# Kernel tuning notes

Hardware: AMD Instinct MI355X
Metric: run time of the kernel (lower is better)

The kernel has to match this reference:

```python
import jax, jax.numpy as jnp
import numpy as np

DIM = 2048
HEADS = 16
DIM_HEAD = 128
DIM_INNER = HEADS * DIM_HEAD  # 2048
EPS = 1.1920929e-07  # torch RMSNorm default eps = finfo(float32).eps


def setup_inputs() -> dict:
    key = jax.random.key(0)
    k_tok, k_q, k_kv, k_o = jax.random.split(key, 4)
    tokens = jax.random.normal(k_tok, (4, 2048, DIM), dtype=jnp.float32)
    # Linear weights stored as [in, out]; torch init ~ U(-1/sqrt(in), 1/sqrt(in)), use scaled normal
    s = 0.02
    w_q = jax.random.normal(k_q, (DIM, DIM_INNER), dtype=jnp.float32) * s
    w_kv = jax.random.normal(k_kv, (DIM, 2 * DIM_INNER), dtype=jnp.float32) * s
    w_out = jax.random.normal(k_o, (DIM_INNER, DIM), dtype=jnp.float32) * s
    norm_weight = jnp.ones((DIM,), dtype=jnp.float32)
    return {"tokens": tokens, "norm_weight": norm_weight, "w_q": w_q, "w_kv": w_kv, "w_out": w_out}


def _rmsnorm(x, weight):
    var = jnp.mean(jnp.square(x), axis=-1, keepdims=True)
    return x * jax.lax.rsqrt(var + EPS) * weight


def reference(tokens, norm_weight, w_q, w_kv, w_out):
    b, n, _ = tokens.shape
    x = _rmsnorm(tokens, norm_weight)
    q = x @ w_q                       # [b, n, h*d]
    kv = x @ w_kv                     # [b, n, 2*h*d]
    k, v = jnp.split(kv, 2, axis=-1)

    def split_heads(t):
        return t.reshape(b, n, HEADS, DIM_HEAD).transpose(0, 2, 1, 3)  # b h n d

    q, k, v = map(split_heads, (q, k, v))
    q = q * (DIM_HEAD ** -0.5)
    sim = jnp.einsum('bhid,bhjd->bhij', q, k)
    attn = jax.nn.softmax(sim, axis=-1)
    out = jnp.einsum('bhij,bhjd->bhid', attn, v)
    out = out.transpose(0, 2, 1, 3).reshape(b, n, DIM_INNER)
    return out @ w_out
```

## Files before the change

### kernel.cpp

```cpp
#include <hip/hip_runtime.h>
#include <hip/hip_bf16.h>
#include <stdint.h>

#define SEQ   2048
#define DIM   2048
#define HEADS 16
#define DHEAD 128
#define BATCH 4
#define MROWS (BATCH*SEQ)

typedef short bf16x8 __attribute__((ext_vector_type(8)));
typedef float f32x4  __attribute__((ext_vector_type(4)));
typedef float f32x16 __attribute__((ext_vector_type(16)));
typedef unsigned short u16x8 __attribute__((ext_vector_type(8)));
typedef unsigned int u32x4 __attribute__((ext_vector_type(4)));

__device__ __forceinline__ short f2bf(float f){
  union { float fv; unsigned u; } x; x.fv = f;
  unsigned r = x.u + 0x7fffu + ((x.u >> 16) & 1u);
  return (short)(r >> 16);
}

__device__ __forceinline__ unsigned cvtpk(float lo, float hi){
  unsigned r; asm("v_cvt_pk_bf16_f32 %0, %1, %2" : "=v"(r) : "v"(lo), "v"(hi)); return r;
}

__device__ __forceinline__ float exp2a(float x){
#if __has_builtin(__builtin_amdgcn_exp2f)
  return __builtin_amdgcn_exp2f(x);
#else
  return exp2f(x);
#endif
}

__device__ __forceinline__ void gl_lds16(const void* g, void* l){
  __builtin_amdgcn_global_load_lds((const __attribute__((address_space(1))) void*)g,
                                   (__attribute__((address_space(3))) void*)l, 16, 0, 0);
}

__global__ __launch_bounds__(256) void rmsnorm_cast_k(const float* __restrict__ tok,
                                                      const float* __restrict__ w,
                                                      short* __restrict__ x){
  const int row = blockIdx.x;
  const float4* r4 = (const float4*)(tok + (size_t)row * DIM);
  float4 a = r4[threadIdx.x * 2];
  float4 b = r4[threadIdx.x * 2 + 1];
  float ss = a.x*a.x + a.y*a.y + a.z*a.z + a.w*a.w
           + b.x*b.x + b.y*b.y + b.z*b.z + b.w*b.w;
  #pragma unroll
  for (int m = 1; m < 64; m <<= 1) ss += __shfl_xor(ss, m, 64);
  __shared__ float red[4];
  if ((threadIdx.x & 63) == 0) red[threadIdx.x >> 6] = ss;
  __syncthreads();
  float tot = red[0] + red[1] + red[2] + red[3];
  float rs = rsqrtf(tot * (1.0f / DIM) + 1.1920929e-07f);
  const float4* w4 = (const float4*)w;
  float4 wa = w4[threadIdx.x * 2];
  float4 wb = w4[threadIdx.x * 2 + 1];
  u16x8 o;
  o[0] = (unsigned short)f2bf(a.x * rs * wa.x);
  o[1] = (unsigned short)f2bf(a.y * rs * wa.y);
  o[2] = (unsigned short)f2bf(a.z * rs * wa.z);
  o[3] = (unsigned short)f2bf(a.w * rs * wa.w);
  o[4] = (unsigned short)f2bf(b.x * rs * wb.x);
  o[5] = (unsigned short)f2bf(b.y * rs * wb.y);
  o[6] = (unsigned short)f2bf(b.z * rs * wb.z);
  o[7] = (unsigned short)f2bf(b.w * rs * wb.w);
  *(u16x8*)(x + (size_t)row * DIM + threadIdx.x * 8) = o;
}

__global__ __launch_bounds__(256) void wtrans_k(const float* __restrict__ w,
                                                short* __restrict__ wt,
                                                int K, int N){
  __shared__ float tile[64][65];
  const int r0 = blockIdx.y * 64;
  const int c0 = blockIdx.x * 64;
  const int t = threadIdx.x;
  #pragma unroll
  for (int i = 0; i < 16; i++){
    int e = i * 256 + t; int r = e >> 6, c = e & 63;
    tile[r][c] = w[(size_t)(r0 + r) * N + c0 + c];
  }
  __syncthreads();
  #pragma unroll
  for (int i = 0; i < 16; i++){
    int e = i * 256 + t; int c = e >> 6, r = e & 63;
    wt[(size_t)(c0 + c) * K + r0 + r] = f2bf(tile[r][c]);
  }
}

__global__ __launch_bounds__(256) void vtrans_k(const short* __restrict__ kv,
                                                short* __restrict__ vt){
  __shared__ short tile[64][65];
  const int n0 = blockIdx.x * 64;
  const int d0 = blockIdx.y * 64;
  const int bh = blockIdx.z;
  const int b = bh >> 4, h = bh & 15;
  const int t = threadIdx.x;
  #pragma unroll
  for (int i = 0; i < 16; i++){
    int e = i * 256 + t; int r = e >> 6, c = e & 63;
    tile[r][c] = kv[(size_t)(b * SEQ + n0 + r) * 4096 + 2048 + h * DHEAD + d0 + c];
  }
  __syncthreads();
  #pragma unroll
  for (int i = 0; i < 16; i++){
    int e = i * 256 + t; int c = e >> 6, r = e & 63;
    vt[(size_t)(bh * DHEAD + d0 + c) * SEQ + n0 + r] = tile[r][c];
  }
}

__device__ __forceinline__ void storeC(float* C, size_t idx, float v){ C[idx] = v; }
__device__ __forceinline__ void storeC(short* C, size_t idx, float v){ C[idx] = f2bf(v); }

template<typename OutT>
__global__ __launch_bounds__(512, 2) void gemm256_k(const short* __restrict__ A,
                                                    const short* __restrict__ Bt,
                                                    OutT* __restrict__ C,
                                                    int M, int N, int K, int lgntn){
  __shared__ __align__(16) short As[4][256 * 32];
  __shared__ __align__(16) short Bs[4][256 * 32];
  const int nwg = gridDim.x;
  const int bid = blockIdx.x;
  const int o = (bid & 7) * (nwg >> 3) + (bid >> 3);
  const int bm = o >> lgntn, bn = o & ((1 << lgntn) - 1);
  const int m0 = bm << 8, n0 = bn << 8;
  const int tid = threadIdx.x, lane = tid & 63, wid = tid >> 6;
  const int l31 = lane & 31, hi = lane >> 5;
  const int wr = wid >> 2, wc = wid & 3;
  const int NT = K >> 5;

  f32x16 acc[4][2] = {};

  auto stage = [&](int t){
    const int slot = t & 3;
    const size_t kbase = (size_t)t << 5;
    #pragma unroll
    for (int i = 0; i < 2; i++){
      int c = i * 512 + tid;
      int row = c >> 2;
      int j = (c & 3) ^ ((row >> 1) & 3);
      gl_lds16(A + (size_t)(m0 + row) * K + kbase + j * 8,
               &As[slot][(i * 512 + wid * 64) * 8]);
    }
    #pragma unroll
    for (int i = 0; i < 2; i++){
      int c = i * 512 + tid;
      int row = c >> 2;
      int j = (c & 3) ^ ((row >> 1) & 3);
      gl_lds16(Bt + (size_t)(n0 + row) * K + kbase + j * 8,
               &Bs[slot][(i * 512 + wid * 64) * 8]);
    }
  };

  auto compute = [&](int t){
    const short* Ab = As[t & 3];
    const short* Bb = Bs[t & 3];
    bf16x8 af[4][2], bfv[2][2];
    #pragma unroll
    for (int mb = 0; mb < 4; mb++){
      int row = wr * 128 + mb * 32 + l31;
      #pragma unroll
      for (int ks = 0; ks < 2; ks++){
        int ch = (ks * 2 + hi) ^ ((row >> 1) & 3);
        af[mb][ks] = *(const bf16x8*)&Ab[row * 32 + ch * 8];
      }
    }
    #pragma unroll
    for (int nb = 0; nb < 2; nb++){
      int row = wc * 64 + nb * 32 + l31;
      #pragma unroll
      for (int ks = 0; ks < 2; ks++){
        int ch = (ks * 2 + hi) ^ ((row >> 1) & 3);
        bfv[nb][ks] = *(const bf16x8*)&Bb[row * 32 + ch * 8];
      }
    }
    __builtin_amdgcn_s_setprio(1);
    #pragma unroll
    for (int mb = 0; mb < 4; mb++)
      #pragma unroll
      for (int nb = 0; nb < 2; nb++)
        #pragma unroll
        for (int ks = 0; ks < 2; ks++)
          acc[mb][nb] = __builtin_amdgcn_mfma_f32_32x32x16_bf16(af[mb][ks], bfv[nb][ks],
                                                                acc[mb][nb], 0, 0, 0);
    __builtin_amdgcn_s_setprio(0);
  };

  stage(0); stage(1); stage(2);
  asm volatile("s_waitcnt vmcnt(8)" ::: "memory");
  __builtin_amdgcn_s_barrier();

  for (int t = 0; t < NT; t++){
    if (t + 3 < NT) stage(t + 3);
    compute(t);
    if (t + 1 < NT){
      if (t + 3 < NT)      asm volatile("s_waitcnt vmcnt(8)" ::: "memory");
      else if (t + 2 < NT) asm volatile("s_waitcnt vmcnt(4)" ::: "memory");
      else                 asm volatile("s_waitcnt vmcnt(0)" ::: "memory");
      __builtin_amdgcn_s_barrier();
    }
  }

  #pragma unroll
  for (int mb = 0; mb < 4; mb++)
    #pragma unroll
    for (int nb = 0; nb < 2; nb++)
      #pragma unroll
      for (int reg = 0; reg < 16; reg++){
        int r = (reg & 3) + 8 * (reg >> 2) + 4 * hi;
        int row = m0 + wr * 128 + mb * 32 + r;
        int col = n0 + wc * 64 + nb * 32 + l31;
        storeC(C, (size_t)row * N + col, acc[mb][nb][reg]);
      }
}

__global__ __launch_bounds__(256) void attn_k(const short* __restrict__ q,
                                              const short* __restrict__ kv,
                                              const short* __restrict__ vt,
                                              short* __restrict__ out){
  __shared__ __align__(16) short Ks[2][64 * 128];
  __shared__ __align__(16) short Vts[2][128 * 64];
  const int qt = blockIdx.x, bh = blockIdx.y;
  const int b = bh >> 4, h = bh & 15;
  const int tid = threadIdx.x, lane = tid & 63, wid = tid >> 6;
  const int l31 = lane & 31, hi = lane >> 5;
  const int qrow0 = qt * 128 + wid * 32;
  const float c2 = 0.08838834764831845f * 1.4426950408889634f;
  const int NT = SEQ / 64;

  bf16x8 qf[8];
  {
    const short* qp = q + (size_t)(b * SEQ + qrow0 + l31) * DIM + h * DHEAD + hi * 8;
    #pragma unroll
    for (int s = 0; s < 8; s++) qf[s] = *(const bf16x8*)(qp + s * 16);
  }

  f32x16 acc[4] = {};
  float m2 = -3e38f, l_s = 0.f;

  auto stage = [&](int kt, int bs){
    #pragma unroll
    for (int i = 0; i < 4; i++){
      int cb = (i * 4 + wid) * 64;
      int c  = cb + lane;
      int kr = c >> 4, kj = (c & 15) ^ (kr & 7);
      gl_lds16(kv + (size_t)(b * SEQ + kt * 64 + kr) * 4096 + h * DHEAD + kj * 8,
               &Ks[bs][cb * 8]);
      int vr = c >> 3, vj = (c & 7) ^ (vr & 7);
      gl_lds16(vt + (size_t)(bh * DHEAD + vr) * SEQ + kt * 64 + vj * 8,
               &Vts[bs][cb * 8]);
    }
  };

  stage(0, 0);
  int cur = 0;

  for (int kt = 0; kt < NT; kt++){
    if (kt + 1 < NT){
      stage(kt + 1, cur ^ 1);
      asm volatile("s_waitcnt vmcnt(8)" ::: "memory");
    } else {
      asm volatile("s_waitcnt vmcnt(0)" ::: "memory");
    }
    __builtin_amdgcn_s_barrier();

    const short* Kb = Ks[cur];
    const short* Vb = Vts[cur];

    f32x16 t0 = {0,0,0,0,0,0,0,0,0,0,0,0,0,0,0,0};
    f32x16 t1 = t0;
    {
      const int r0 = l31, r1 = l31 + 32;
      #pragma unroll
      for (int s = 0; s < 8; s++){
        bf16x8 k0 = *(const bf16x8*)&Kb[r0 * 128 + (((2 * s + hi) ^ (r0 & 7)) * 8)];
        bf16x8 k1 = *(const bf16x8*)&Kb[r1 * 128 + (((2 * s + hi) ^ (r1 & 7)) * 8)];
        t0 = __builtin_amdgcn_mfma_f32_32x32x16_bf16(k0, qf[s], t0, 0, 0, 0);
        t1 = __builtin_amdgcn_mfma_f32_32x32x16_bf16(k1, qf[s], t1, 0, 0, 0);
      }
    }

    float mxr = t0[0];
    #pragma unroll
    for (int i = 1; i < 16; i++) mxr = fmaxf(mxr, t0[i]);
    #pragma unroll
    for (int i = 0; i < 16; i++) mxr = fmaxf(mxr, t1[i]);
    mxr = fmaxf(mxr, __shfl_xor(mxr, 32));
    float mx2 = mxr * c2;
    if (!__all(mx2 <= m2 + 11.5f)){
      float m2n = fmaxf(m2, mx2);
      float al = exp2a(m2 - m2n);
      m2 = m2n;
      l_s *= al;
      #pragma unroll
      for (int reg = 0; reg < 16; reg++){
        float ar = __shfl(al, (reg & 3) + 8 * (reg >> 2) + 4 * hi);
        #pragma unroll
        for (int dt = 0; dt < 4; dt++) acc[dt][reg] *= ar;
      }
    }

    float ps = 0.f;
    unsigned w[16];
    #pragma unroll
    for (int pr = 0; pr < 8; pr++){
      float pa_ = exp2a(fmaf(t0[2 * pr], c2, -m2));
      float pb_ = exp2a(fmaf(t0[2 * pr + 1], c2, -m2));
      ps += pa_ + pb_;
      w[pr] = cvtpk(pa_, pb_);
    }
    #pragma unroll
    for (int pr = 0; pr < 8; pr++){
      float pa_ = exp2a(fmaf(t1[2 * pr], c2, -m2));
      float pb_ = exp2a(fmaf(t1[2 * pr + 1], c2, -m2));
      ps += pa_ + pb_;
      w[8 + pr] = cvtpk(pa_, pb_);
    }
    ps += __shfl_xor(ps, 32);
    l_s += ps;

    #pragma unroll
    for (int fp = 0; fp < 4; fp++){
      unsigned A0 = w[fp * 4 + 0], A1 = w[fp * 4 + 1];
      unsigned B0 = w[fp * 4 + 2], B1 = w[fp * 4 + 3];
      unsigned xA0 = __shfl_xor((int)A0, 32), xA1 = __shfl_xor((int)A1, 32);
      unsigned xB0 = __shfl_xor((int)B0, 32), xB1 = __shfl_xor((int)B1, 32);
      u32x4 fw;
      fw[0] = hi ? xB0 : A0;
      fw[1] = hi ? xB1 : A1;
      fw[2] = hi ? B0 : xA0;
      fw[3] = hi ? B1 : xA1;
      union { u32x4 u; bf16x8 v; } pc; pc.u = fw;
      #pragma unroll
      for (int dt = 0; dt < 4; dt++){
        int vr = dt * 32 + l31;
        bf16x8 vb = *(const bf16x8*)&Vb[vr * 64 + (((2 * fp + hi) ^ (vr & 7)) * 8)];
        acc[dt] = __builtin_amdgcn_mfma_f32_32x32x16_bf16(pc.v, vb, acc[dt], 0, 0, 0);
      }
    }

    asm volatile("s_waitcnt lgkmcnt(0)" ::: "memory");
    __builtin_amdgcn_s_barrier();
    cur ^= 1;
  }

  float inv = 1.0f / l_s;
  #pragma unroll
  for (int reg = 0; reg < 16; reg++){
    int cr = (reg & 3) + 8 * (reg >> 2) + 4 * hi;
    float li = __shfl(inv, cr);
    int row = qrow0 + cr;
    #pragma unroll
    for (int dt = 0; dt < 4; dt++)
      out[(size_t)(b * SEQ + row) * DIM + h * DHEAD + dt * 32 + l31] = f2bf(acc[dt][reg] * li);
  }
}

extern "C" void kernel_launch(void* const* d_in, const int* in_sizes, int n_in,
                              void* d_out, int out_size, void* d_ws, size_t ws_size,
                              hipStream_t stream) {
  (void)in_sizes; (void)n_in; (void)out_size; (void)ws_size;
  const float* tokens = (const float*)d_in[0];
  const float* normw  = (const float*)d_in[1];
  const float* wq     = (const float*)d_in[2];
  const float* wkv    = (const float*)d_in[3];
  const float* wout   = (const float*)d_in[4];
  float* outp = (float*)d_out;
  char* ws = (char*)d_ws;

  short* x     = (short*)(ws + 0);
  short* wqt   = (short*)(ws + 33554432);
  short* wkvt  = (short*)(ws + 41943040);
  short* woutt = (short*)(ws + 58720256);
  short* qb    = (short*)(ws + 67108864);
  short* kvb   = (short*)(ws + 100663296);
  short* vtb   = (short*)(ws + 167772160);

  rmsnorm_cast_k<<<dim3(MROWS), dim3(256), 0, stream>>>(tokens, normw, x);
  wtrans_k<<<dim3(2048/64, 2048/64), dim3(256), 0, stream>>>(wq,   wqt,   2048, 2048);
  wtrans_k<<<dim3(4096/64, 2048/64), dim3(256), 0, stream>>>(wkv,  wkvt,  2048, 4096);
  wtrans_k<<<dim3(2048/64, 2048/64), dim3(256), 0, stream>>>(wout, woutt, 2048, 2048);
  gemm256_k<short><<<dim3((MROWS/256)*(2048/256)), dim3(512), 0, stream>>>(x, wqt,  qb,  MROWS, 2048, 2048, 3);
  gemm256_k<short><<<dim3((MROWS/256)*(4096/256)), dim3(512), 0, stream>>>(x, wkvt, kvb, MROWS, 4096, 2048, 4);
  vtrans_k<<<dim3(SEQ/64, DHEAD/64, BATCH*HEADS), dim3(256), 0, stream>>>(kvb, vtb);
  attn_k<<<dim3(SEQ/128, BATCH*HEADS), dim3(256), 0, stream>>>(qb, kvb, vtb, qb);
  gemm256_k<float><<<dim3((MROWS/256)*(2048/256)), dim3(512), 0, stream>>>(qb, woutt, outp, MROWS, 2048, 2048, 3);
}
```

Measured before the change: 610.9 us.

## Restage attention K/V loads with single-buffered V and add scheduling fences

The attention loop now loads the current V tile at the start of each iteration and prefetches the next K tile, with V kept in a single LDS buffer. The wait-and-barrier moves to just before the PV MFMAs, so V loads overlap the QK product and softmax. This cuts attention LDS use, which could allow more resident blocks, in exchange for a full vmcnt(0) drain at the end of each iteration. Separately, sched_barrier fences are added around GEMM and attention staging, the row-max becomes a tree reduction, and the exp sums are split across four accumulators to shorten dependency chains.

Result: slower. 649.3 us (+6.3%).

```diff
diff --git a/kernel.cpp b/kernel.cpp
--- a/kernel.cpp
+++ b/kernel.cpp
@@ -36,6 +36,11 @@
 __device__ __forceinline__ void gl_lds16(const void* g, void* l){
   __builtin_amdgcn_global_load_lds((const __attribute__((address_space(1))) void*)g,
                                    (__attribute__((address_space(3))) void*)l, 16, 0, 0);
+}
+
+__device__ __forceinline__ void ofence(){
+  asm volatile("" ::: "memory");
+  __builtin_amdgcn_sched_barrier(0);
 }
 
 __global__ __launch_bounds__(256) void rmsnorm_cast_k(const float* __restrict__ tok,
@@ -187,12 +192,14 @@
     __builtin_amdgcn_s_setprio(0);
   };
 
-  stage(0); stage(1); stage(2);
+  stage(0); ofence();
+  stage(1); ofence();
+  stage(2); ofence();
   asm volatile("s_waitcnt vmcnt(8)" ::: "memory");
   __builtin_amdgcn_s_barrier();
 
   for (int t = 0; t < NT; t++){
-    if (t + 3 < NT) stage(t + 3);
+    if (t + 3 < NT){ stage(t + 3); ofence(); }
     compute(t);
     if (t + 1 < NT){
       if (t + 3 < NT)      asm volatile("s_waitcnt vmcnt(8)" ::: "memory");
@@ -220,7 +227,7 @@
                                               const short* __restrict__ vt,
                                               short* __restrict__ out){
   __shared__ __align__(16) short Ks[2][64 * 128];
-  __shared__ __align__(16) short Vts[2][128 * 64];
+  __shared__ __align__(16) short Vts[128 * 64];
   const int qt = blockIdx.x, bh = blockIdx.y;
   const int b = bh >> 4, h = bh & 15;
   const int tid = threadIdx.x, lane = tid & 63, wid = tid >> 6;
@@ -235,11 +242,12 @@
     #pragma unroll
     for (int s = 0; s < 8; s++) qf[s] = *(const bf16x8*)(qp + s * 16);
   }
+  ofence();
 
   f32x16 acc[4] = {};
   float m2 = -3e38f, l_s = 0.f;
 
-  auto stage = [&](int kt, int bs){
+  auto stage_K = [&](int kt, int bs){
     #pragma unroll
     for (int i = 0; i < 4; i++){
       int cb = (i * 4 + wid) * 64;
@@ -247,26 +255,31 @@
       int kr = c >> 4, kj = (c & 15) ^ (kr & 7);
       gl_lds16(kv + (size_t)(b * SEQ + kt * 64 + kr) * 4096 + h * DHEAD + kj * 8,
                &Ks[bs][cb * 8]);
+    }
+  };
+  auto stage_V = [&](int kt){
+    #pragma unroll
+    for (int i = 0; i < 4; i++){
+      int cb = (i * 4 + wid) * 64;
+      int c  = cb + lane;
       int vr = c >> 3, vj = (c & 7) ^ (vr & 7);
       gl_lds16(vt + (size_t)(bh * DHEAD + vr) * SEQ + kt * 64 + vj * 8,
-               &Vts[bs][cb * 8]);
+               &Vts[cb * 8]);
     }
   };
 
-  stage(0, 0);
-  int cur = 0;
+  stage_K(0, 0); ofence();
 
   for (int kt = 0; kt < NT; kt++){
-    if (kt + 1 < NT){
-      stage(kt + 1, cur ^ 1);
+    const int cur = kt & 1;
+    stage_V(kt); ofence();
+    if (kt + 1 < NT){ stage_K(kt + 1, cur ^ 1); ofence(); }
+    if (kt == 0){
       asm volatile("s_waitcnt vmcnt(8)" ::: "memory");
-    } else {
-      asm volatile("s_waitcnt vmcnt(0)" ::: "memory");
-    }
-    __builtin_amdgcn_s_barrier();
+      __builtin_amdgcn_s_barrier();
+    }
 
     const short* Kb = Ks[cur];
-    const short* Vb = Vts[cur];
 
     f32x16 t0 = {0,0,0,0,0,0,0,0,0,0,0,0,0,0,0,0};
     f32x16 t1 = t0;
@@ -281,12 +294,15 @@
       }
     }
 
-    float mxr = t0[0];
-    #pragma unroll
-    for (int i = 1; i < 16; i++) mxr = fmaxf(mxr, t0[i]);
-    #pragma unroll
-    for (int i = 0; i < 16; i++) mxr = fmaxf(mxr, t1[i]);
-    mxr = fmaxf(mxr, __shfl_xor(mxr, 32));
+    float mr[8];
+    #pragma unroll
+    for (int i = 0; i < 8; i++)
+      mr[i] = fmaxf(fmaxf(t0[i], t0[i + 8]), fmaxf(t1[i], t1[i + 8]));
+    #pragma unroll
+    for (int s = 4; s > 0; s >>= 1)
+      #pragma unroll
+      for (int i = 0; i < s; i++) mr[i] = fmaxf(mr[i], mr[i + s]);
+    float mxr = fmaxf(mr[0], __shfl_xor(mr[0], 32));
     float mx2 = mxr * c2;
     if (!__all(mx2 <= m2 + 11.5f)){
       float m2n = fmaxf(m2, mx2);
@@ -301,24 +317,29 @@
       }
     }
 
-    float ps = 0.f;
+    float ps0 = 0.f, ps1 = 0.f, ps2 = 0.f, ps3 = 0.f;
     unsigned w[16];
     #pragma unroll
     for (int pr = 0; pr < 8; pr++){
       float pa_ = exp2a(fmaf(t0[2 * pr], c2, -m2));
       float pb_ = exp2a(fmaf(t0[2 * pr + 1], c2, -m2));
-      ps += pa_ + pb_;
+      ps0 += pa_; ps1 += pb_;
       w[pr] = cvtpk(pa_, pb_);
     }
     #pragma unroll
     for (int pr = 0; pr < 8; pr++){
       float pa_ = exp2a(fmaf(t1[2 * pr], c2, -m2));
       float pb_ = exp2a(fmaf(t1[2 * pr + 1], c2, -m2));
-      ps += pa_ + pb_;
+      ps2 += pa_; ps3 += pb_;
       w[8 + pr] = cvtpk(pa_, pb_);
     }
+    float ps = (ps0 + ps1) + (ps2 + ps3);
     ps += __shfl_xor(ps, 32);
     l_s += ps;
+
+    if (kt + 1 < NT) asm volatile("s_waitcnt vmcnt(4)" ::: "memory");
+    else             asm volatile("s_waitcnt vmcnt(0)" ::: "memory");
+    __builtin_amdgcn_s_barrier();
 
     #pragma unroll
     for (int fp = 0; fp < 4; fp++){
@@ -335,14 +356,13 @@
       #pragma unroll
       for (int dt = 0; dt < 4; dt++){
         int vr = dt * 32 + l31;
-        bf16x8 vb = *(const bf16x8*)&Vb[vr * 64 + (((2 * fp + hi) ^ (vr & 7)) * 8)];
+        bf16x8 vb = *(const bf16x8*)&Vts[vr * 64 + (((2 * fp + hi) ^ (vr & 7)) * 8)];
         acc[dt] = __builtin_amdgcn_mfma_f32_32x32x16_bf16(pc.v, vb, acc[dt], 0, 0, 0);
       }
     }
 
-    asm volatile("s_waitcnt lgkmcnt(0)" ::: "memory");
+    asm volatile("s_waitcnt vmcnt(0) lgkmcnt(0)" ::: "memory");
     __builtin_amdgcn_s_barrier();
-    cur ^= 1;
   }
 
   float inv = 1.0f / l_s;
```

## Process two query tiles per wave in attention to share K/V fragment loads

Applied to the files above, without the earlier changes.

Each attention wave now handles 64 query rows as two 32-row tiles. Every K and V fragment read from LDS feeds two MFMA chains, which halves LDS traffic per unit of matrix work. The online softmax now runs per 32-key subtile for each query tile, and the grid is halved to match. Scheduling barriers are also added around the async stage loads in the GEMM and attention kernels to pin instruction order. The cost is much higher register use (two sets of accumulators and Q fragments) and half as many blocks, which may lower occupancy or cause spills.

Result: slower. 624.0 us (+2.1%).

```diff
diff --git a/kernel.cpp b/kernel.cpp
--- a/kernel.cpp
+++ b/kernel.cpp
@@ -36,6 +36,11 @@
 __device__ __forceinline__ void gl_lds16(const void* g, void* l){
   __builtin_amdgcn_global_load_lds((const __attribute__((address_space(1))) void*)g,
                                    (__attribute__((address_space(3))) void*)l, 16, 0, 0);
+}
+
+__device__ __forceinline__ void ofence(){
+  asm volatile("" ::: "memory");
+  __builtin_amdgcn_sched_barrier(0);
 }
 
 __global__ __launch_bounds__(256) void rmsnorm_cast_k(const float* __restrict__ tok,
@@ -187,12 +192,14 @@
     __builtin_amdgcn_s_setprio(0);
   };
 
-  stage(0); stage(1); stage(2);
+  stage(0); ofence();
+  stage(1); ofence();
+  stage(2); ofence();
   asm volatile("s_waitcnt vmcnt(8)" ::: "memory");
   __builtin_amdgcn_s_barrier();
 
   for (int t = 0; t < NT; t++){
-    if (t + 3 < NT) stage(t + 3);
+    if (t + 3 < NT){ stage(t + 3); ofence(); }
     compute(t);
     if (t + 1 < NT){
       if (t + 3 < NT)      asm volatile("s_waitcnt vmcnt(8)" ::: "memory");
@@ -225,19 +232,22 @@
   const int b = bh >> 4, h = bh & 15;
   const int tid = threadIdx.x, lane = tid & 63, wid = tid >> 6;
   const int l31 = lane & 31, hi = lane >> 5;
-  const int qrow0 = qt * 128 + wid * 32;
+  const int qrow0 = qt * 256 + wid * 64;
   const float c2 = 0.08838834764831845f * 1.4426950408889634f;
   const int NT = SEQ / 64;
 
-  bf16x8 qf[8];
+  bf16x8 qfA[8], qfB[8];
   {
-    const short* qp = q + (size_t)(b * SEQ + qrow0 + l31) * DIM + h * DHEAD + hi * 8;
-    #pragma unroll
-    for (int s = 0; s < 8; s++) qf[s] = *(const bf16x8*)(qp + s * 16);
-  }
-
-  f32x16 acc[4] = {};
-  float m2 = -3e38f, l_s = 0.f;
+    const short* qpA = q + (size_t)(b * SEQ + qrow0 + l31) * DIM + h * DHEAD + hi * 8;
+    const short* qpB = qpA + (size_t)32 * DIM;
+    #pragma unroll
+    for (int s = 0; s < 8; s++){ qfA[s] = *(const bf16x8*)(qpA + s * 16);
+                                 qfB[s] = *(const bf16x8*)(qpB + s * 16); }
+  }
+  ofence();
+
+  f32x16 accA[4] = {}, accB[4] = {};
+  float m2A = -3e38f, lA = 0.f, m2B = -3e38f, lB = 0.f;
 
   auto stage = [&](int kt, int bs){
     #pragma unroll
@@ -253,12 +263,47 @@
     }
   };
 
-  stage(0, 0);
-  int cur = 0;
+  auto smpack = [&](f32x16& t, float& m2r, float& lr, f32x16* acc_, unsigned* wv){
+    float mr[8];
+    #pragma unroll
+    for (int i = 0; i < 8; i++) mr[i] = fmaxf(t[i], t[i + 8]);
+    #pragma unroll
+    for (int s = 4; s > 0; s >>= 1)
+      #pragma unroll
+      for (int i = 0; i < s; i++) mr[i] = fmaxf(mr[i], mr[i + s]);
+    float mxr = fmaxf(mr[0], __shfl_xor(mr[0], 32));
+    float mx2 = mxr * c2;
+    if (!__all(mx2 <= m2r + 11.5f)){
+      float m2n = fmaxf(m2r, mx2);
+      float al = exp2a(m2r - m2n);
+      m2r = m2n;
+      lr *= al;
+      #pragma unroll
+      for (int reg = 0; reg < 16; reg++){
+        float ar = __shfl(al, (reg & 3) + 8 * (reg >> 2) + 4 * hi);
+        #pragma unroll
+        for (int dt = 0; dt < 4; dt++) acc_[dt][reg] *= ar;
+      }
+    }
+    float p0 = 0.f, p1 = 0.f;
+    #pragma unroll
+    for (int pr = 0; pr < 8; pr++){
+      float pa_ = exp2a(fmaf(t[2 * pr], c2, -m2r));
+      float pb_ = exp2a(fmaf(t[2 * pr + 1], c2, -m2r));
+      p0 += pa_; p1 += pb_;
+      wv[pr] = cvtpk(pa_, pb_);
+    }
+    float ps = p0 + p1;
+    ps += __shfl_xor(ps, 32);
+    lr += ps;
+  };
+
+  stage(0, 0); ofence();
 
   for (int kt = 0; kt < NT; kt++){
+    const int cur = kt & 1;
     if (kt + 1 < NT){
-      stage(kt + 1, cur ^ 1);
+      stage(kt + 1, cur ^ 1); ofence();
       asm volatile("s_waitcnt vmcnt(8)" ::: "memory");
     } else {
       asm volatile("s_waitcnt vmcnt(0)" ::: "memory");
@@ -268,92 +313,72 @@
     const short* Kb = Ks[cur];
     const short* Vb = Vts[cur];
 
-    f32x16 t0 = {0,0,0,0,0,0,0,0,0,0,0,0,0,0,0,0};
-    f32x16 t1 = t0;
-    {
-      const int r0 = l31, r1 = l31 + 32;
-      #pragma unroll
-      for (int s = 0; s < 8; s++){
-        bf16x8 k0 = *(const bf16x8*)&Kb[r0 * 128 + (((2 * s + hi) ^ (r0 & 7)) * 8)];
-        bf16x8 k1 = *(const bf16x8*)&Kb[r1 * 128 + (((2 * s + hi) ^ (r1 & 7)) * 8)];
-        t0 = __builtin_amdgcn_mfma_f32_32x32x16_bf16(k0, qf[s], t0, 0, 0, 0);
-        t1 = __builtin_amdgcn_mfma_f32_32x32x16_bf16(k1, qf[s], t1, 0, 0, 0);
-      }
-    }
-
-    float mxr = t0[0];
-    #pragma unroll
-    for (int i = 1; i < 16; i++) mxr = fmaxf(mxr, t0[i]);
-    #pragma unroll
-    for (int i = 0; i < 16; i++) mxr = fmaxf(mxr, t1[i]);
-    mxr = fmaxf(mxr, __shfl_xor(mxr, 32));
-    float mx2 = mxr * c2;
-    if (!__all(mx2 <= m2 + 11.5f)){
-      float m2n = fmaxf(m2, mx2);
-      float al = exp2a(m2 - m2n);
-      m2 = m2n;
-      l_s *= al;
-      #pragma unroll
-      for (int reg = 0; reg < 16; reg++){
-        float ar = __shfl(al, (reg & 3) + 8 * (reg >> 2) + 4 * hi);
+    #pragma unroll
+    for (int ksub = 0; ksub < 2; ksub++){
+      f32x16 tA = {0,0,0,0,0,0,0,0,0,0,0,0,0,0,0,0};
+      f32x16 tB = tA;
+      {
+        const int r = ksub * 32 + l31;
+        __builtin_amdgcn_s_setprio(1);
         #pragma unroll
-        for (int dt = 0; dt < 4; dt++) acc[dt][reg] *= ar;
-      }
-    }
-
-    float ps = 0.f;
-    unsigned w[16];
-    #pragma unroll
-    for (int pr = 0; pr < 8; pr++){
-      float pa_ = exp2a(fmaf(t0[2 * pr], c2, -m2));
-      float pb_ = exp2a(fmaf(t0[2 * pr + 1], c2, -m2));
-      ps += pa_ + pb_;
-      w[pr] = cvtpk(pa_, pb_);
-    }
-    #pragma unroll
-    for (int pr = 0; pr < 8; pr++){
-      float pa_ = exp2a(fmaf(t1[2 * pr], c2, -m2));
-      float pb_ = exp2a(fmaf(t1[2 * pr + 1], c2, -m2));
-      ps += pa_ + pb_;
-      w[8 + pr] = cvtpk(pa_, pb_);
-    }
-    ps += __shfl_xor(ps, 32);
-    l_s += ps;
-
-    #pragma unroll
-    for (int fp = 0; fp < 4; fp++){
-      unsigned A0 = w[fp * 4 + 0], A1 = w[fp * 4 + 1];
-      unsigned B0 = w[fp * 4 + 2], B1 = w[fp * 4 + 3];
-      unsigned xA0 = __shfl_xor((int)A0, 32), xA1 = __shfl_xor((int)A1, 32);
-      unsigned xB0 = __shfl_xor((int)B0, 32), xB1 = __shfl_xor((int)B1, 32);
-      u32x4 fw;
-      fw[0] = hi ? xB0 : A0;
-      fw[1] = hi ? xB1 : A1;
-      fw[2] = hi ? B0 : xA0;
-      fw[3] = hi ? B1 : xA1;
-      union { u32x4 u; bf16x8 v; } pc; pc.u = fw;
-      #pragma unroll
-      for (int dt = 0; dt < 4; dt++){
-        int vr = dt * 32 + l31;
-        bf16x8 vb = *(const bf16x8*)&Vb[vr * 64 + (((2 * fp + hi) ^ (vr & 7)) * 8)];
-        acc[dt] = __builtin_amdgcn_mfma_f32_32x32x16_bf16(pc.v, vb, acc[dt], 0, 0, 0);
+        for (int s = 0; s < 8; s++){
+          bf16x8 k = *(const bf16x8*)&Kb[r * 128 + (((2 * s + hi) ^ (r & 7)) * 8)];
+          tA = __builtin_amdgcn_mfma_f32_32x32x16_bf16(k, qfA[s], tA, 0, 0, 0);
+          tB = __builtin_amdgcn_mfma_f32_32x32x16_bf16(k, qfB[s], tB, 0, 0, 0);
+        }
+        __builtin_amdgcn_s_setprio(0);
+      }
+
+      unsigned wA[8], wB[8];
+      smpack(tA, m2A, lA, accA, wA);
+      smpack(tB, m2B, lB, accB, wB);
+
+      #pragma unroll
+      for (int fpl = 0; fpl < 2; fpl++){
+        unsigned A0 = wA[fpl * 4 + 0], A1 = wA[fpl * 4 + 1];
+        unsigned B0 = wA[fpl * 4 + 2], B1 = wA[fpl * 4 + 3];
+        unsigned xA0 = __shfl_xor((int)A0, 32), xA1 = __shfl_xor((int)A1, 32);
+        unsigned xB0 = __shfl_xor((int)B0, 32), xB1 = __shfl_xor((int)B1, 32);
+        u32x4 fwA;
+        fwA[0] = hi ? xB0 : A0;  fwA[1] = hi ? xB1 : A1;
+        fwA[2] = hi ? B0 : xA0;  fwA[3] = hi ? B1 : xA1;
+        unsigned C0 = wB[fpl * 4 + 0], C1 = wB[fpl * 4 + 1];
+        unsigned D0 = wB[fpl * 4 + 2], D1 = wB[fpl * 4 + 3];
+        unsigned xC0 = __shfl_xor((int)C0, 32), xC1 = __shfl_xor((int)C1, 32);
+        unsigned xD0 = __shfl_xor((int)D0, 32), xD1 = __shfl_xor((int)D1, 32);
+        u32x4 fwB;
+        fwB[0] = hi ? xD0 : C0;  fwB[1] = hi ? xD1 : C1;
+        fwB[2] = hi ? D0 : xC0;  fwB[3] = hi ? D1 : xC1;
+        union { u32x4 u; bf16x8 v; } pA, pB; pA.u = fwA; pB.u = fwB;
+        const int fp = ksub * 2 + fpl;
+        __builtin_amdgcn_s_setprio(1);
+        #pragma unroll
+        for (int dt = 0; dt < 4; dt++){
+          int vr = dt * 32 + l31;
+          bf16x8 vb = *(const bf16x8*)&Vb[vr * 64 + (((2 * fp + hi) ^ (vr & 7)) * 8)];
+          accA[dt] = __builtin_amdgcn_mfma_f32_32x32x16_bf16(pA.v, vb, accA[dt], 0, 0, 0);
+          accB[dt] = __builtin_amdgcn_mfma_f32_32x32x16_bf16(pB.v, vb, accB[dt], 0, 0, 0);
+        }
+        __builtin_amdgcn_s_setprio(0);
       }
     }
 
     asm volatile("s_waitcnt lgkmcnt(0)" ::: "memory");
     __builtin_amdgcn_s_barrier();
-    cur ^= 1;
-  }
-
-  float inv = 1.0f / l_s;
+  }
+
+  float invA = 1.0f / lA, invB = 1.0f / lB;
   #pragma unroll
   for (int reg = 0; reg < 16; reg++){
     int cr = (reg & 3) + 8 * (reg >> 2) + 4 * hi;
-    float li = __shfl(inv, cr);
-    int row = qrow0 + cr;
-    #pragma unroll
-    for (int dt = 0; dt < 4; dt++)
-      out[(size_t)(b * SEQ + row) * DIM + h * DHEAD + dt * 32 + l31] = f2bf(acc[dt][reg] * li);
+    float liA = __shfl(invA, cr);
+    float liB = __shfl(invB, cr);
+    int rowA = qrow0 + cr;
+    #pragma unroll
+    for (int dt = 0; dt < 4; dt++){
+      out[(size_t)(b * SEQ + rowA) * DIM + h * DHEAD + dt * 32 + l31] = f2bf(accA[dt][reg] * liA);
+      out[(size_t)(b * SEQ + rowA + 32) * DIM + h * DHEAD + dt * 32 + l31] = f2bf(accB[dt][reg] * liB);
+    }
   }
 }
 
@@ -384,6 +409,6 @@
   gemm256_k<short><<<dim3((MROWS/256)*(2048/256)), dim3(512), 0, stream>>>(x, wqt,  qb,  MROWS, 2048, 2048, 3);
   gemm256_k<short><<<dim3((MROWS/256)*(4096/256)), dim3(512), 0, stream>>>(x, wkvt, kvb, MROWS, 4096, 2048, 4);
   vtrans_k<<<dim3(SEQ/64, DHEAD/64, BATCH*HEADS), dim3(256), 0, stream>>>(kvb, vtb);
-  attn_k<<<dim3(SEQ/128, BATCH*HEADS), dim3(256), 0, stream>>>(qb, kvb, vtb, qb);
+  attn_k<<<dim3(SEQ/256, BATCH*HEADS), dim3(256), 0, stream>>>(qb, kvb, vtb, qb);
   gemm256_k<float><<<dim3((MROWS/256)*(2048/256)), dim3(512), 0, stream>>>(qb, woutt, outp, MROWS, 2048, 2048, 3);
 }
```

## Split GEMM k-step into two phases interleaving A/B prefetch with MFMA halves

Applied to the files above, without the earlier changes.

Restructures the 256x256 GEMM main loop into two half-steps. Each half loads a subset of A fragments from LDS, issues either the A or the B global-to-LDS prefetch for stage t+3, hits a barrier, then runs half of the MFMAs. Scheduling fences keep the compiler from merging or reordering the phases. The goal is to interleave memory issue with matrix work and spread LDS reads, in the style of a ping-pong schedule, at the cost of extra barriers per k-step.

Measured after the change: 589.6 us. -3.5%, faster.

```diff
diff --git a/kernel.cpp b/kernel.cpp
--- a/kernel.cpp
+++ b/kernel.cpp
@@ -36,6 +36,11 @@
 __device__ __forceinline__ void gl_lds16(const void* g, void* l){
   __builtin_amdgcn_global_load_lds((const __attribute__((address_space(1))) void*)g,
                                    (__attribute__((address_space(3))) void*)l, 16, 0, 0);
+}
+
+__device__ __forceinline__ void ofence(){
+  asm volatile("" ::: "memory");
+  __builtin_amdgcn_sched_barrier(0);
 }
 
 __global__ __launch_bounds__(256) void rmsnorm_cast_k(const float* __restrict__ tok,
@@ -132,7 +137,7 @@
 
   f32x16 acc[4][2] = {};
 
-  auto stage = [&](int t){
+  auto stageA = [&](int t){
     const int slot = t & 3;
     const size_t kbase = (size_t)t << 5;
     #pragma unroll
@@ -143,6 +148,10 @@
       gl_lds16(A + (size_t)(m0 + row) * K + kbase + j * 8,
                &As[slot][(i * 512 + wid * 64) * 8]);
     }
+  };
+  auto stageB = [&](int t){
+    const int slot = t & 3;
+    const size_t kbase = (size_t)t << 5;
     #pragma unroll
     for (int i = 0; i < 2; i++){
       int c = i * 512 + tid;
@@ -153,19 +162,17 @@
     }
   };
 
-  auto compute = [&](int t){
+  stageA(0); stageB(0); ofence();
+  stageA(1); stageB(1); ofence();
+  stageA(2); stageB(2); ofence();
+  asm volatile("s_waitcnt vmcnt(8)" ::: "memory");
+  __builtin_amdgcn_s_barrier();
+
+  for (int t = 0; t < NT; t++){
     const short* Ab = As[t & 3];
     const short* Bb = Bs[t & 3];
-    bf16x8 af[4][2], bfv[2][2];
-    #pragma unroll
-    for (int mb = 0; mb < 4; mb++){
-      int row = wr * 128 + mb * 32 + l31;
-      #pragma unroll
-      for (int ks = 0; ks < 2; ks++){
-        int ch = (ks * 2 + hi) ^ ((row >> 1) & 3);
-        af[mb][ks] = *(const bf16x8*)&Ab[row * 32 + ch * 8];
-      }
-    }
+
+    bf16x8 bfv[2][2], af0[2][2];
     #pragma unroll
     for (int nb = 0; nb < 2; nb++){
       int row = wc * 64 + nb * 32 + l31;
@@ -175,25 +182,51 @@
         bfv[nb][ks] = *(const bf16x8*)&Bb[row * 32 + ch * 8];
       }
     }
+    #pragma unroll
+    for (int mb = 0; mb < 2; mb++){
+      int row = wr * 128 + mb * 32 + l31;
+      #pragma unroll
+      for (int ks = 0; ks < 2; ks++){
+        int ch = (ks * 2 + hi) ^ ((row >> 1) & 3);
+        af0[mb][ks] = *(const bf16x8*)&Ab[row * 32 + ch * 8];
+      }
+    }
+    if (t + 3 < NT){ stageA(t + 3); ofence(); }
+    __builtin_amdgcn_s_barrier();
     __builtin_amdgcn_s_setprio(1);
     #pragma unroll
-    for (int mb = 0; mb < 4; mb++)
+    for (int mb = 0; mb < 2; mb++)
       #pragma unroll
       for (int nb = 0; nb < 2; nb++)
         #pragma unroll
         for (int ks = 0; ks < 2; ks++)
-          acc[mb][nb] = __builtin_amdgcn_mfma_f32_32x32x16_bf16(af[mb][ks], bfv[nb][ks],
-                                                                acc[mb][nb], 0, 0, 0);
+          acc[mb][nb] = __builtin_amdgcn_mfma_f32_32x32x16_bf16(af0[mb][ks], bfv[nb][ks],
+                                                               acc[mb][nb], 0, 0, 0);
     __builtin_amdgcn_s_setprio(0);
-  };
-
-  stage(0); stage(1); stage(2);
-  asm volatile("s_waitcnt vmcnt(8)" ::: "memory");
-  __builtin_amdgcn_s_barrier();
-
-  for (int t = 0; t < NT; t++){
-    if (t + 3 < NT) stage(t + 3);
-    compute(t);
+
+    bf16x8 af1[2][2];
+    #pragma unroll
+    for (int mb = 0; mb < 2; mb++){
+      int row = wr * 128 + (mb + 2) * 32 + l31;
+      #pragma unroll
+      for (int ks = 0; ks < 2; ks++){
+        int ch = (ks * 2 + hi) ^ ((row >> 1) & 3);
+        af1[mb][ks] = *(const bf16x8*)&Ab[row * 32 + ch * 8];
+      }
+    }
+    if (t + 3 < NT){ stageB(t + 3); ofence(); }
+    __builtin_amdgcn_s_barrier();
+    __builtin_amdgcn_s_setprio(1);
+    #pragma unroll
+    for (int mb = 0; mb < 2; mb++)
+      #pragma unroll
+      for (int nb = 0; nb < 2; nb++)
+        #pragma unroll
+        for (int ks = 0; ks < 2; ks++)
+          acc[mb + 2][nb] = __builtin_amdgcn_mfma_f32_32x32x16_bf16(af1[mb][ks], bfv[nb][ks],
+                                                                   acc[mb + 2][nb], 0, 0, 0);
+    __builtin_amdgcn_s_setprio(0);
+
     if (t + 1 < NT){
       if (t + 3 < NT)      asm volatile("s_waitcnt vmcnt(8)" ::: "memory");
       else if (t + 2 < NT) asm volatile("s_waitcnt vmcnt(4)" ::: "memory");
```
